# Kernel tuning notes

Hardware: AMD Instinct MI355X
Metric: run time of the kernel (lower is better)

The kernel has to match this reference:

```python
import jax, jax.numpy as jnp
import numpy as np

B, S, D = 64, 14, 2048   # batch, enc_image_size, encoder_dim
A, H, E = 512, 512, 512  # attention_dim, lstm_size, embedding_size
V, L = 10000, 20         # vocab_size, max caption length (T = L-1 decode steps)


def setup_inputs() -> dict:
    key = jax.random.key(0)
    ks = jax.random.split(key, 24)
    p = lambda k, shape: jax.random.normal(k, shape, jnp.float32) * 0.02
    features = jax.random.normal(ks[0], (B, S, S, D), jnp.float32)
    captions = jax.random.randint(ks[1], (B, L), 0, V)
    # sorted descending lengths in [2, L], max forced to L so T_dec = L-1
    lengths = jnp.sort(jax.random.randint(ks[2], (B,), 2, L + 1))[::-1]
    lengths = lengths.at[0].set(L)
    return {
        'features': features, 'captions': captions, 'lengths': lengths,
        'emb': p(ks[3], (V, E)),
        'W_ih': p(ks[4], (4 * H, D + E)), 'b_ih': p(ks[5], (4 * H,)),
        'W_hh': p(ks[6], (4 * H, H)), 'b_hh': p(ks[7], (4 * H,)),
        'h_fc_w': p(ks[8], (H, D)), 'h_fc_b': p(ks[9], (H,)),
        'c_fc_w': p(ks[10], (H, D)), 'c_fc_b': p(ks[11], (H,)),
        'f_beta_w': p(ks[12], (D, H)), 'f_beta_b': p(ks[13], (D,)),
        'cls_w': p(ks[14], (V, H)), 'cls_b': p(ks[15], (V,)),
        'enc_w': p(ks[16], (A, D)), 'enc_b': p(ks[17], (A,)),
        'dec_w': p(ks[18], (A, H)), 'dec_b': p(ks[19], (A,)),
        'att_w': p(ks[20], (1, A)), 'att_b': p(ks[21], (1,)),
    }


def reference(features, captions, lengths, emb, W_ih, b_ih, W_hh, b_hh,
              h_fc_w, h_fc_b, c_fc_w, c_fc_b, f_beta_w, f_beta_b,
              cls_w, cls_b, enc_w, enc_b, dec_w, dec_b, att_w, att_b):
    feats = features.reshape(features.shape[0], -1, features.shape[-1])  # (B,P,D)
    emb_seq = emb[captions]                                              # (B,L,E)
    mean_f = feats.mean(axis=1)
    h = mean_f @ h_fc_w.T + h_fc_b
    c = mean_f @ c_fc_w.T + c_fc_b
    dec_len = lengths - 1
    T = captions.shape[1] - 1
    # attention encoder projection is time-invariant: hoist out of the loop
    att1 = jnp.einsum('bpd,ad->bpa', feats, enc_w) + enc_b               # (B,P,A)

    def step(carry, xs):
        h, c = carry
        x_emb, t = xs
        att2 = h @ dec_w.T + dec_b                                       # (B,A)
        e = jnp.einsum('bpa,a->bp', jax.nn.relu(att1 + att2[:, None, :]), att_w[0]) + att_b[0]
        alpha = jax.nn.softmax(e, axis=1)                                # (B,P)
        awe = jnp.einsum('bp,bpd->bd', alpha, feats)
        gate = jax.nn.sigmoid(h @ f_beta_w.T + f_beta_b)
        awe = gate * awe
        x = jnp.concatenate([x_emb, awe], axis=1)                        # (B,E+D)
        gates = x @ W_ih.T + b_ih + h @ W_hh.T + b_hh                    # torch gate order i,f,g,o
        i, f, g, o = jnp.split(gates, 4, axis=1)
        c2 = jax.nn.sigmoid(f) * c + jax.nn.sigmoid(i) * jnp.tanh(g)
        h2 = jax.nn.sigmoid(o) * jnp.tanh(c2)
        y = h2 @ cls_w.T + cls_b                                         # dropout = eval identity
        active = (t < dec_len)[:, None]
        return (h2, c2), (jnp.where(active, y, 0.0), jnp.where(active, alpha, 0.0))

    xs = (jnp.swapaxes(emb_seq[:, :T], 0, 1), jnp.arange(T))
    (_, _), (y_pred, alphas) = jax.lax.scan(step, (h, c), xs)
    return jnp.swapaxes(y_pred, 0, 1), jnp.swapaxes(alphas, 0, 1)
```

## Files before the change

### kernel.cpp

```cpp
#include <hip/hip_runtime.h>
#include <math.h>

typedef __attribute__((ext_vector_type(8))) short bf16x8;
typedef __attribute__((ext_vector_type(8))) unsigned short u16x8;
typedef __attribute__((ext_vector_type(4))) float f32x4;

#define NB 64
#define NP 196
#define ND 2048
#define NA 512
#define NH 512
#define NE 512
#define NV 10000
#define NT 19
#define NROW (NB*NP)
#define NVP 10112
#define MROW 1280
#define NHP 4608

__device__ __forceinline__ unsigned short f2bu(float f){
    unsigned int u; __builtin_memcpy(&u, &f, 4);
    u = (u + 0x7FFFu + ((u >> 16) & 1u)) >> 16;
    return (unsigned short)u;
}
__device__ __forceinline__ float b2f(unsigned short s){
    unsigned int u = ((unsigned int)s) << 16;
    float f; __builtin_memcpy(&f, &u, 4); return f;
}
__device__ __forceinline__ float sigm(float x){ return 1.f/(1.f + __expf(-x)); }

__device__ __forceinline__ void gll16(const void* g, void* l){
    __builtin_amdgcn_global_load_lds(
        (const __attribute__((address_space(1))) void*)g,
        (__attribute__((address_space(3))) void*)l, 16, 0, 0);
}


__global__ void k_prep(const float4* __restrict__ enc_w, const float4* __restrict__ dec_w,
                       const float4* __restrict__ f_beta_w, const float4* __restrict__ W_ih,
                       const float4* __restrict__ W_hh, const float4* __restrict__ h_fc_w,
                       const float4* __restrict__ c_fc_w, const float4* __restrict__ cls_w,
                       ushort4* __restrict__ encwb, ushort4* __restrict__ whp,
                       ushort4* __restrict__ wgates, ushort4* __restrict__ wembb,
                       ushort4* __restrict__ whc, ushort4* __restrict__ clswb,
                       ushort4* __restrict__ hsb_pad){
    const int n0 = NA*ND/4;
    const int n1 = NHP*512/4;
    const int n2 = 2048*2048/4;
    const int n3 = 2048*512/4;
    const int n4 = 1024*2048/4;
    const int n5 = NVP*NH/4;
    const int n6 = 64*512/4;
    const int total = n0+n1+n2+n3+n4+n5+n6;
    int stride = gridDim.x*blockDim.x;
    for (int i = blockIdx.x*blockDim.x + threadIdx.x; i < total; i += stride){
        int idx = i;
        float4 v; ushort4 o;
        if (idx < n0){
            v = enc_w[idx];
            o.x = f2bu(v.x); o.y = f2bu(v.y); o.z = f2bu(v.z); o.w = f2bu(v.w);
            encwb[idx] = o; continue;
        }
        idx -= n0;
        if (idx < n1){
            if (idx < 512*512/4) v = dec_w[idx];
            else if (idx < 2560*512/4) v = f_beta_w[idx - 512*512/4];
            else v = W_hh[idx - 2560*512/4];
            o.x = f2bu(v.x); o.y = f2bu(v.y); o.z = f2bu(v.z); o.w = f2bu(v.w);
            whp[idx] = o; continue;
        }
        idx -= n1;
        if (idx < n2){
            int j = idx >> 9, kk4 = idx & 511;
            v = W_ih[(size_t)j*640 + 128 + kk4];
            o.x = f2bu(v.x); o.y = f2bu(v.y); o.z = f2bu(v.z); o.w = f2bu(v.w);
            wgates[idx] = o; continue;
        }
        idx -= n2;
        if (idx < n3){
            int j = idx >> 7, kk4 = idx & 127;
            v = W_ih[(size_t)j*640 + kk4];
            o.x = f2bu(v.x); o.y = f2bu(v.y); o.z = f2bu(v.z); o.w = f2bu(v.w);
            wembb[idx] = o; continue;
        }
        idx -= n3;
        if (idx < n4){
            v = (idx < 512*2048/4) ? h_fc_w[idx] : c_fc_w[idx - 512*2048/4];
            o.x = f2bu(v.x); o.y = f2bu(v.y); o.z = f2bu(v.z); o.w = f2bu(v.w);
            whc[idx] = o; continue;
        }
        idx -= n4;
        if (idx < n5){
            if (idx < NV*NH/4){
                v = cls_w[idx];
                o.x = f2bu(v.x); o.y = f2bu(v.y); o.z = f2bu(v.z); o.w = f2bu(v.w);
            } else { o.x = 0; o.y = 0; o.z = 0; o.w = 0; }
            clswb[idx] = o; continue;
        }
        idx -= n5;
        o.x = 0; o.y = 0; o.z = 0; o.w = 0;
        hsb_pad[idx] = o;
    }
}

__global__ void __launch_bounds__(1024) k_cm(const float* __restrict__ feats,
                                             unsigned short* __restrict__ fbf,
                                             unsigned short* __restrict__ meanbf){
    __shared__ float4 msum[1024];
    int dc = blockIdx.x;
    int b  = blockIdx.y;
    int tid = threadIdx.x;
    int c4 = tid & 63;
    int rq = tid >> 6;
    int D0 = dc*256;
    float4 acc = {0.f,0.f,0.f,0.f};
    for (int p = rq; p < NP; p += 16){
        float4 v = *(const float4*)(feats + ((size_t)(b*NP + p))*ND + D0 + c4*4);
        acc.x += v.x; acc.y += v.y; acc.z += v.z; acc.w += v.w;
        ushort4 u4;
        u4.x = f2bu(v.x); u4.y = f2bu(v.y); u4.z = f2bu(v.z); u4.w = f2bu(v.w);
        *(ushort4*)(fbf + ((size_t)(b*NP + p))*ND + D0 + c4*4) = u4;
    }
    msum[tid] = acc;
    __syncthreads();
    if (tid < 64){
        float4 tot = {0.f,0.f,0.f,0.f};
        #pragma unroll
        for (int k = 0; k < 16; k++){
            float4 s = msum[tid + 64*k];
            tot.x += s.x; tot.y += s.y; tot.z += s.z; tot.w += s.w;
        }
        ushort4 o;
        o.x = f2bu(tot.x*(1.f/196.f)); o.y = f2bu(tot.y*(1.f/196.f));
        o.z = f2bu(tot.z*(1.f/196.f)); o.w = f2bu(tot.w*(1.f/196.f));
        *(ushort4*)(meanbf + (size_t)b*ND + D0 + tid*4) = o;
    }
}

__global__ void k_embg(const float* __restrict__ emb, const int* __restrict__ captions,
                       unsigned short* __restrict__ embcat){
    int blk = blockIdx.x, tid = threadIdx.x;
    int r = blk*4 + (tid >> 6);
    int cg = tid & 63;
    u16x8 o;
    #pragma unroll
    for (int k = 0; k < 8; k++) o[k] = 0;
    if (r < NT*64){
        int t = r >> 6, b = r & 63;
        int tok = captions[b*20 + t];
        const float* e = emb + (size_t)tok*NE + cg*8;
        float4 v0 = *(const float4*)e;
        float4 v1 = *(const float4*)(e + 4);
        o[0] = f2bu(v0.x); o[1] = f2bu(v0.y); o[2] = f2bu(v0.z); o[3] = f2bu(v0.w);
        o[4] = f2bu(v1.x); o[5] = f2bu(v1.y); o[6] = f2bu(v1.z); o[7] = f2bu(v1.w);
    }
    *(u16x8*)(embcat + (size_t)r*NE + cg*8) = o;
}

__global__ void k_hc0m(const unsigned short* __restrict__ meanbf,
                       const unsigned short* __restrict__ whc,
                       const float* __restrict__ h_fc_b, const float* __restrict__ c_fc_b,
                       unsigned short* __restrict__ hbf, float* __restrict__ cst){
    int tid = threadIdx.x;
    int w = tid >> 6, l = tid & 63;
    int nt = blockIdx.x;
    int row = 16*w + (l & 15);
    int col = nt*16 + (l & 15);
    int kg = (l >> 4) * 8;
    f32x4 acc = {};
    for (int k0 = 0; k0 < ND; k0 += 32){
        bf16x8 af = *(const bf16x8*)(meanbf + (size_t)row*ND + k0 + kg);
        bf16x8 bv = *(const bf16x8*)(whc + (size_t)col*ND + k0 + kg);
        acc = __builtin_amdgcn_mfma_f32_16x16x32_bf16(af, bv, acc, 0, 0, 0);
    }
    int r0 = 16*w + (l >> 4)*4;
    #pragma unroll
    for (int r = 0; r < 4; r++){
        int b = r0 + r;
        if (col < 512) hbf[b*NH + col] = f2bu(acc[r] + h_fc_b[col]);
        else           cst[b*NH + (col - 512)] = acc[r] + c_fc_b[col - 512];
    }
}

template<int K>
__device__ __forceinline__ void gemm128(const unsigned short* __restrict__ A,
                                        const unsigned short* __restrict__ B,
                                        int brow, int bcol, f32x4 acc[4][4]){
    __shared__ unsigned short As[128*32];
    __shared__ unsigned short Bs[128*32];
    int tid = threadIdx.x;
    int w = tid >> 6, l = tid & 63;
    int wr = (w >> 1) * 64, wc = (w & 1) * 64;
    int lr = l & 15, kg = (l >> 4) * 8;
    const unsigned short* ga0 = A + (size_t)(brow + (tid >> 2))*K + (tid & 3)*8;
    const unsigned short* gb0 = B + (size_t)(bcol + (tid >> 2))*K + (tid & 3)*8;
    for (int k0 = 0; k0 < K; k0 += 32){
        __syncthreads();
        gll16(ga0 + k0,                As + w*512);
        gll16(ga0 + (size_t)64*K + k0, As + 2048 + w*512);
        gll16(gb0 + k0,                Bs + w*512);
        gll16(gb0 + (size_t)64*K + k0, Bs + 2048 + w*512);
        __syncthreads();
        bf16x8 af[4], bfr[4];
        #pragma unroll
        for (int mi = 0; mi < 4; mi++)
            af[mi] = *(const bf16x8*)(As + (wr + mi*16 + lr)*32 + kg);
        #pragma unroll
        for (int ni = 0; ni < 4; ni++)
            bfr[ni] = *(const bf16x8*)(Bs + (wc + ni*16 + lr)*32 + kg);
        #pragma unroll
        for (int ni = 0; ni < 4; ni++){
            #pragma unroll
            for (int mi = 0; mi < 4; mi++)
                acc[mi][ni] = __builtin_amdgcn_mfma_f32_16x16x32_bf16(af[mi], bfr[ni], acc[mi][ni], 0, 0, 0);
        }
    }
}

__global__ void k_gemm_att1(const unsigned short* __restrict__ fbf,
                            const unsigned short* __restrict__ encw,
                            const float* __restrict__ enc_b,
                            unsigned short* __restrict__ att1){
    f32x4 acc[4][4] = {};
    int brow = blockIdx.y*128, bcol = blockIdx.x*128;
    gemm128<ND>(fbf, encw, brow, bcol, acc);
    int w = threadIdx.x >> 6, l = threadIdx.x & 63;
    int wr = (w >> 1) * 64, wc = (w & 1) * 64;
    int r0 = brow + wr + (l >> 4)*4;
    int c0 = bcol + wc + (l & 15);
    #pragma unroll
    for (int ni = 0; ni < 4; ni++){
        int col = c0 + ni*16;
        float eb = enc_b[col];
        #pragma unroll
        for (int mi = 0; mi < 4; mi++){
            #pragma unroll
            for (int r = 0; r < 4; r++)
                att1[(size_t)(r0 + mi*16 + r)*NA + col] = f2bu(acc[mi][ni][r] + eb);
        }
    }
}

__global__ void k_gemb(const unsigned short* __restrict__ embcat,
                       const unsigned short* __restrict__ wembb,
                       const float* __restrict__ b_ih, const float* __restrict__ b_hh,
                       float* __restrict__ gemb){
    f32x4 acc[4][4] = {};
    int brow = blockIdx.x*128, bcol = blockIdx.y*128;
    gemm128<NE>(embcat, wembb, brow, bcol, acc);
    int w = threadIdx.x >> 6, l = threadIdx.x & 63;
    int wr = (w >> 1) * 64, wc = (w & 1) * 64;
    int r0 = brow + wr + (l >> 4)*4;
    int c0 = bcol + wc + (l & 15);
    #pragma unroll
    for (int ni = 0; ni < 4; ni++){
        int col = c0 + ni*16;
        float bias = b_ih[col] + b_hh[col];
        #pragma unroll
        for (int mi = 0; mi < 4; mi++){
            #pragma unroll
            for (int r = 0; r < 4; r++)
                gemb[(size_t)(r0 + mi*16 + r)*2048 + col] = acc[mi][ni][r] + bias;
        }
    }
}

__global__ void k_gemm_cls(const unsigned short* __restrict__ hsb,
                           const unsigned short* __restrict__ clsw,
                           const float* __restrict__ cls_b,
                           const int* __restrict__ lengths,
                           float* __restrict__ yout){
    f32x4 acc[4][4] = {};
    int brow = blockIdx.x*128, bcol = blockIdx.y*128;
    gemm128<NH>(hsb, clsw, brow, bcol, acc);
    int w = threadIdx.x >> 6, l = threadIdx.x & 63;
    int wr = (w >> 1) * 64, wc = (w & 1) * 64;
    int r0 = brow + wr + (l >> 4)*4;
    int c0 = bcol + wc + (l & 15);
    #pragma unroll
    for (int ni = 0; ni < 4; ni++){
        int col = c0 + ni*16;
        if (col >= NV) continue;
        float cb = cls_b[col];
        #pragma unroll
        for (int mi = 0; mi < 4; mi++){
            #pragma unroll
            for (int r = 0; r < 4; r++){
                int grow = r0 + mi*16 + r;
                if (grow >= NT*64) continue;
                int t = grow >> 6, bb = grow & 63;
                int active = t < (lengths[bb] - 1);
                yout[((size_t)bb*NT + t)*NV + col] = active ? (acc[mi][ni][r] + cb) : 0.f;
            }
        }
    }
}


__global__ void k_hall(const unsigned short* __restrict__ hbf,
                       const unsigned short* __restrict__ whp,
                       const float* __restrict__ dec_b, const float* __restrict__ f_beta_b,
                       float* __restrict__ hp){
    int w = threadIdx.x >> 6, l = threadIdx.x & 63;
    int nt = blockIdx.x;
    int row = 16*w + (l & 15);
    int col = nt*16 + (l & 15);
    int kg = (l >> 4) * 8;
    f32x4 acc = {};
    for (int k0 = 0; k0 < NH; k0 += 32){
        bf16x8 af = *(const bf16x8*)(hbf + row*NH + k0 + kg);
        bf16x8 bv = *(const bf16x8*)(whp + (size_t)col*NH + k0 + kg);
        acc = __builtin_amdgcn_mfma_f32_16x16x32_bf16(af, bv, acc, 0, 0, 0);
    }
    int r0 = 16*w + (l >> 4)*4;
    float bias = (col < 512) ? dec_b[col] : f_beta_b[col - 512];
    #pragma unroll
    for (int r = 0; r < 4; r++)
        hp[(size_t)(r0 + r)*NHP + col] = acc[r] + bias;
}

__global__ void k_e(const unsigned short* __restrict__ att1,
                    const float* __restrict__ hp,
                    const float* __restrict__ att_w, const float* __restrict__ att_b,
                    float* __restrict__ ews){
    __shared__ float at2[NA];
    __shared__ float aw[NA];
    int b = blockIdx.x >> 2, pc = blockIdx.x & 3;
    int tid = threadIdx.x;
    for (int j = tid; j < NA; j += 256){
        at2[j] = hp[(size_t)b*NHP + j];
        aw[j]  = att_w[j];
    }
    __syncthreads();
    int pl = tid >> 2, q = tid & 3;
    if (pl < 49){
        int p = pc*49 + pl;
        const unsigned short* arow = att1 + ((size_t)(b*NP + p))*NA + q*128;
        float s = 0.f;
        for (int a0 = 0; a0 < 128; a0 += 8){
            bf16x8 v = *(const bf16x8*)(arow + a0);
            #pragma unroll
            for (int e = 0; e < 8; e++){
                int ai = q*128 + a0 + e;
                float x = b2f((unsigned short)v[e]) + at2[ai];
                s += fmaxf(x, 0.f) * aw[ai];
            }
        }
        s += __shfl_xor(s, 1);
        s += __shfl_xor(s, 2);
        if (q == 0) ews[b*NP + p] = s + att_b[0];
    }
}

__global__ void k_awe(const float* __restrict__ ews, const unsigned short* __restrict__ fbf,
                      const float* __restrict__ hp, const int* __restrict__ lengths,
                      unsigned short* __restrict__ xg, float* __restrict__ alphas, int t){
    __shared__ float al[NP];
    __shared__ float red[256];
    int dc = blockIdx.x;
    int b  = blockIdx.y;
    int tid = threadIdx.x;
    float v = (tid < NP) ? ews[b*NP + tid] : -1e30f;
    red[tid] = v; __syncthreads();
    for (int s = 128; s > 0; s >>= 1){ if (tid < s) red[tid] = fmaxf(red[tid], red[tid+s]); __syncthreads(); }
    float m = red[0]; __syncthreads();
    float ev = (tid < NP) ? __expf(v - m) : 0.f;
    red[tid] = ev; __syncthreads();
    for (int s = 128; s > 0; s >>= 1){ if (tid < s) red[tid] += red[tid+s]; __syncthreads(); }
    float inv = 1.f / red[0];
    if (tid < NP) al[tid] = ev * inv;
    __syncthreads();
    if (dc == 0 && tid < NP){
        int active = t < (lengths[b] - 1);
        alphas[((size_t)b*NT + t)*NP + tid] = active ? al[tid] : 0.f;
    }
    int d = dc*256 + tid;
    const unsigned short* fb = fbf + (size_t)(b*NP)*ND + d;
    float a0 = 0.f, a1 = 0.f, a2 = 0.f, a3 = 0.f;
    for (int p = 0; p < 196; p += 4){
        a0 += al[p]     * b2f(fb[(size_t)p*ND]);
        a1 += al[p + 1] * b2f(fb[(size_t)(p + 1)*ND]);
        a2 += al[p + 2] * b2f(fb[(size_t)(p + 2)*ND]);
        a3 += al[p + 3] * b2f(fb[(size_t)(p + 3)*ND]);
    }
    float accv = (a0 + a1) + (a2 + a3);
    float g = sigm(hp[(size_t)b*NHP + 512 + d]);
    xg[b*2048 + d] = f2bu(g * accv);
}

__global__ void k_glstm(const unsigned short* __restrict__ xg,
                        const unsigned short* __restrict__ hin,
                        const unsigned short* __restrict__ whp,
                        const unsigned short* __restrict__ wgates,
                        const float* __restrict__ gemb,
                        float* __restrict__ cst, unsigned short* __restrict__ hbf,
                        unsigned short* __restrict__ hsb, int t){
    int nt = blockIdx.x;
    int rblk = blockIdx.y;
    int l = threadIdx.x;
    int lr = l & 15;
    int kg = (l >> 4) * 8;
    int a = lr >> 2, g = lr & 3;
    int j  = nt*4 + a;
    int jp = g*512 + j;
    int arow0 = rblk*16 + lr;
    f32x4 acc = {};
    const unsigned short* ax = xg + (size_t)arow0*2048;
    const unsigned short* bx = wgates + (size_t)jp*2048;
    for (int k0 = 0; k0 < 2048; k0 += 32){
        bf16x8 af = *(const bf16x8*)(ax + k0 + kg);
        bf16x8 bv = *(const bf16x8*)(bx + k0 + kg);
        acc = __builtin_amdgcn_mfma_f32_16x16x32_bf16(af, bv, acc, 0, 0, 0);
    }
    const unsigned short* ah = hin + (size_t)arow0*NH;
    const unsigned short* bh = whp + (size_t)(2560 + jp)*NH;
    for (int k0 = 0; k0 < NH; k0 += 32){
        bf16x8 af = *(const bf16x8*)(ah + k0 + kg);
        bf16x8 bv = *(const bf16x8*)(bh + k0 + kg);
        acc = __builtin_amdgcn_mfma_f32_16x16x32_bf16(af, bv, acc, 0, 0, 0);
    }
    const float* ge = gemb + (size_t)t*64*2048;
    #pragma unroll
    for (int rr = 0; rr < 4; rr++){
        int row = rblk*16 + (l >> 4)*4 + rr;
        float gval = acc[rr] + ge[(size_t)row*2048 + jp];
        float vi = __shfl(gval, (l & ~3) + 0);
        float vf = __shfl(gval, (l & ~3) + 1);
        float vg = __shfl(gval, (l & ~3) + 2);
        float vo = __shfl(gval, (l & ~3) + 3);
        if ((l & 3) == 0){
            float cp = cst[row*NH + j];
            float c2 = sigm(vf)*cp + sigm(vi)*tanhf(vg);
            float h2 = sigm(vo)*tanhf(c2);
            cst[row*NH + j] = c2;
            unsigned short u = f2bu(h2);
            hbf[row*NH + j] = u;
            hsb[((size_t)t*64 + row)*NH + j] = u;
        }
    }
}


extern "C" void kernel_launch(void* const* d_in, const int* in_sizes, int n_in,
                              void* d_out, int out_size, void* d_ws, size_t ws_size,
                              hipStream_t stream){
    const float* features = (const float*)d_in[0];
    const int*   captions = (const int*)d_in[1];
    const int*   lengths  = (const int*)d_in[2];
    const float* emb      = (const float*)d_in[3];
    const float* W_ih     = (const float*)d_in[4];
    const float* b_ih     = (const float*)d_in[5];
    const float* W_hh     = (const float*)d_in[6];
    const float* b_hh     = (const float*)d_in[7];
    const float* h_fc_w   = (const float*)d_in[8];
    const float* h_fc_b   = (const float*)d_in[9];
    const float* c_fc_w   = (const float*)d_in[10];
    const float* c_fc_b   = (const float*)d_in[11];
    const float* f_beta_w = (const float*)d_in[12];
    const float* f_beta_b = (const float*)d_in[13];
    const float* cls_w    = (const float*)d_in[14];
    const float* cls_b    = (const float*)d_in[15];
    const float* enc_w    = (const float*)d_in[16];
    const float* enc_b    = (const float*)d_in[17];
    const float* dec_w    = (const float*)d_in[18];
    const float* dec_b    = (const float*)d_in[19];
    const float* att_w    = (const float*)d_in[20];
    const float* att_b    = (const float*)d_in[21];

    char* w = (char*)d_ws;
    size_t off = 0;
    auto alloc = [&](size_t bytes)->char*{
        char* p = w + off;
        off += (bytes + 255) & ~(size_t)255;
        return p;
    };
    unsigned short* fbf    = (unsigned short*)alloc((size_t)NROW*ND*2);
    unsigned short* att1   = (unsigned short*)alloc((size_t)NROW*NA*2);
    unsigned short* encwb  = (unsigned short*)alloc((size_t)NA*ND*2);
    unsigned short* whp    = (unsigned short*)alloc((size_t)NHP*NH*2);
    unsigned short* wgates = (unsigned short*)alloc((size_t)2048*2048*2);
    unsigned short* wembb  = (unsigned short*)alloc((size_t)2048*NE*2);
    unsigned short* whc    = (unsigned short*)alloc((size_t)1024*ND*2);
    unsigned short* clswb  = (unsigned short*)alloc((size_t)NVP*NH*2);
    unsigned short* embcat = (unsigned short*)alloc((size_t)MROW*NE*2);
    unsigned short* hsb    = (unsigned short*)alloc((size_t)MROW*NH*2);
    unsigned short* hbf    = (unsigned short*)alloc((size_t)64*NH*2);
    unsigned short* xg     = (unsigned short*)alloc((size_t)64*2048*2);
    unsigned short* meanbf = (unsigned short*)alloc((size_t)64*ND*2);
    float* gemb  = (float*)alloc((size_t)MROW*2048*4);
    float* cst   = (float*)alloc((size_t)64*NH*4);
    float* hp    = (float*)alloc((size_t)64*NHP*4);
    float* ews   = (float*)alloc((size_t)64*NP*4);

    float* yout = (float*)d_out;
    float* alphas_out = yout + (size_t)NB*NT*NV;

    k_cm<<<dim3(8, 64), 1024, 0, stream>>>(features, fbf, meanbf);
    k_prep<<<2048, 256, 0, stream>>>((const float4*)enc_w, (const float4*)dec_w,
                                     (const float4*)f_beta_w, (const float4*)W_ih,
                                     (const float4*)W_hh, (const float4*)h_fc_w,
                                     (const float4*)c_fc_w, (const float4*)cls_w,
                                     (ushort4*)encwb, (ushort4*)whp, (ushort4*)wgates,
                                     (ushort4*)wembb, (ushort4*)whc, (ushort4*)clswb,
                                     (ushort4*)(hsb + (size_t)NT*64*NH));
    k_embg<<<320, 256, 0, stream>>>(emb, captions, embcat);
    k_hc0m<<<64, 256, 0, stream>>>(meanbf, whc, h_fc_b, c_fc_b, hbf, cst);
    k_gemm_att1<<<dim3(4, 98), 256, 0, stream>>>(fbf, encwb, enc_b, att1);
    k_gemb<<<dim3(10, 16), 256, 0, stream>>>(embcat, wembb, b_ih, b_hh, gemb);

    for (int t = 0; t < NT; t++){
        k_hall<<<160, 256, 0, stream>>>(hbf, whp, dec_b, f_beta_b, hp);
        k_e<<<256, 256, 0, stream>>>(att1, hp, att_w, att_b, ews);
        k_awe<<<dim3(8, 64), 256, 0, stream>>>(ews, fbf, hp, lengths, xg, alphas_out, t);
        k_glstm<<<dim3(128, 4), 64, 0, stream>>>(xg, hbf, whp, wgates, gemb,
                                                 cst, hbf, hsb, t);
    }
    k_gemm_cls<<<dim3(10, 79), 256, 0, stream>>>(hsb, clswb, cls_b, lengths, yout);
}
```

Baseline: 1.032 ms.

## Fuse hidden-state projections into attention-score and weighted-encoding kernels

```diff
diff --git a/kernel.cpp b/kernel.cpp
--- a/kernel.cpp
+++ b/kernel.cpp
@@ -297,39 +297,37 @@
 }
 
 
-__global__ void k_hall(const unsigned short* __restrict__ hbf,
-                       const unsigned short* __restrict__ whp,
-                       const float* __restrict__ dec_b, const float* __restrict__ f_beta_b,
-                       float* __restrict__ hp){
-    int w = threadIdx.x >> 6, l = threadIdx.x & 63;
-    int nt = blockIdx.x;
-    int row = 16*w + (l & 15);
-    int col = nt*16 + (l & 15);
-    int kg = (l >> 4) * 8;
-    f32x4 acc = {};
-    for (int k0 = 0; k0 < NH; k0 += 32){
-        bf16x8 af = *(const bf16x8*)(hbf + row*NH + k0 + kg);
-        bf16x8 bv = *(const bf16x8*)(whp + (size_t)col*NH + k0 + kg);
-        acc = __builtin_amdgcn_mfma_f32_16x16x32_bf16(af, bv, acc, 0, 0, 0);
-    }
-    int r0 = 16*w + (l >> 4)*4;
-    float bias = (col < 512) ? dec_b[col] : f_beta_b[col - 512];
-    #pragma unroll
-    for (int r = 0; r < 4; r++)
-        hp[(size_t)(r0 + r)*NHP + col] = acc[r] + bias;
-}
-
 __global__ void k_e(const unsigned short* __restrict__ att1,
-                    const float* __restrict__ hp,
+                    const unsigned short* __restrict__ hbf,
+                    const unsigned short* __restrict__ whp,
+                    const float* __restrict__ dec_b,
                     const float* __restrict__ att_w, const float* __restrict__ att_b,
                     float* __restrict__ ews){
+    __shared__ float hl[NH];
     __shared__ float at2[NA];
     __shared__ float aw[NA];
     int b = blockIdx.x >> 2, pc = blockIdx.x & 3;
     int tid = threadIdx.x;
-    for (int j = tid; j < NA; j += 256){
-        at2[j] = hp[(size_t)b*NHP + j];
-        aw[j]  = att_w[j];
+    for (int j = tid; j < NH; j += 256) hl[j] = b2f(hbf[b*NH + j]);
+    for (int j = tid; j < NA; j += 256) aw[j] = att_w[j];
+    __syncthreads();
+    #pragma unroll
+    for (int cc = 0; cc < 2; cc++){
+        int col = tid + cc*256;
+        const unsigned short* wr = whp + (size_t)col*NH;
+        float a0 = 0.f, a1 = 0.f, a2 = 0.f, a3 = 0.f;
+        for (int k0 = 0; k0 < NH; k0 += 32){
+            #pragma unroll
+            for (int q = 0; q < 4; q++){
+                bf16x8 v = *(const bf16x8*)(wr + k0 + q*8);
+                float s = 0.f;
+                #pragma unroll
+                for (int e = 0; e < 8; e++) s += hl[k0 + q*8 + e] * b2f((unsigned short)v[e]);
+                if (q == 0) a0 += s; else if (q == 1) a1 += s;
+                else if (q == 2) a2 += s; else a3 += s;
+            }
+        }
+        at2[col] = dec_b[col] + (a0 + a1) + (a2 + a3);
     }
     __syncthreads();
     int pl = tid >> 2, q = tid & 3;
@@ -353,13 +351,18 @@
 }
 
 __global__ void k_awe(const float* __restrict__ ews, const unsigned short* __restrict__ fbf,
-                      const float* __restrict__ hp, const int* __restrict__ lengths,
+                      const unsigned short* __restrict__ hbf,
+                      const unsigned short* __restrict__ whp,
+                      const float* __restrict__ f_beta_b,
+                      const int* __restrict__ lengths,
                       unsigned short* __restrict__ xg, float* __restrict__ alphas, int t){
+    __shared__ float hl[NH];
     __shared__ float al[NP];
     __shared__ float red[256];
     int dc = blockIdx.x;
     int b  = blockIdx.y;
     int tid = threadIdx.x;
+    for (int j = tid; j < NH; j += 256) hl[j] = b2f(hbf[b*NH + j]);
     float v = (tid < NP) ? ews[b*NP + tid] : -1e30f;
     red[tid] = v; __syncthreads();
     for (int s = 128; s > 0; s >>= 1){ if (tid < s) red[tid] = fmaxf(red[tid], red[tid+s]); __syncthreads(); }
@@ -375,6 +378,20 @@
         alphas[((size_t)b*NT + t)*NP + tid] = active ? al[tid] : 0.f;
     }
     int d = dc*256 + tid;
+    const unsigned short* wr = whp + (size_t)(512 + d)*NH;
+    float g0 = 0.f, g1 = 0.f, g2 = 0.f, g3 = 0.f;
+    for (int k0 = 0; k0 < NH; k0 += 32){
+        #pragma unroll
+        for (int q = 0; q < 4; q++){
+            bf16x8 wv = *(const bf16x8*)(wr + k0 + q*8);
+            float s = 0.f;
+            #pragma unroll
+            for (int e = 0; e < 8; e++) s += hl[k0 + q*8 + e] * b2f((unsigned short)wv[e]);
+            if (q == 0) g0 += s; else if (q == 1) g1 += s;
+            else if (q == 2) g2 += s; else g3 += s;
+        }
+    }
+    float g = sigm(f_beta_b[d] + (g0 + g1) + (g2 + g3));
     const unsigned short* fb = fbf + (size_t)(b*NP)*ND + d;
     float a0 = 0.f, a1 = 0.f, a2 = 0.f, a3 = 0.f;
     for (int p = 0; p < 196; p += 4){
@@ -384,7 +401,6 @@
         a3 += al[p + 3] * b2f(fb[(size_t)(p + 3)*ND]);
     }
     float accv = (a0 + a1) + (a2 + a3);
-    float g = sigm(hp[(size_t)b*NHP + 512 + d]);
     xg[b*2048 + d] = f2bu(g * accv);
 }
 
@@ -489,7 +505,6 @@
     unsigned short* meanbf = (unsigned short*)alloc((size_t)64*ND*2);
     float* gemb  = (float*)alloc((size_t)MROW*2048*4);
     float* cst   = (float*)alloc((size_t)64*NH*4);
-    float* hp    = (float*)alloc((size_t)64*NHP*4);
     float* ews   = (float*)alloc((size_t)64*NP*4);
 
     float* yout = (float*)d_out;
@@ -509,9 +524,9 @@
     k_gemb<<<dim3(10, 16), 256, 0, stream>>>(embcat, wembb, b_ih, b_hh, gemb);
 
     for (int t = 0; t < NT; t++){
-        k_hall<<<160, 256, 0, stream>>>(hbf, whp, dec_b, f_beta_b, hp);
-        k_e<<<256, 256, 0, stream>>>(att1, hp, att_w, att_b, ews);
-        k_awe<<<dim3(8, 64), 256, 0, stream>>>(ews, fbf, hp, lengths, xg, alphas_out, t);
+        k_e<<<256, 256, 0, stream>>>(att1, hbf, whp, dec_b, att_w, att_b, ews);
+        k_awe<<<dim3(8, 64), 256, 0, stream>>>(ews, fbf, hbf, whp, f_beta_b,
+                                               lengths, xg, alphas_out, t);
         k_glstm<<<dim3(128, 4), 64, 0, stream>>>(xg, hbf, whp, wgates, gemb,
                                                  cst, hbf, hsb, t);
     }
```

Result: slower. 1.587 ms (+53.8%).
